# Kernel tuning notes

Measured on AMD Instinct MI355X. Metric: run time of the kernel, lower is better.

Reference implementation:

```python
import jax, jax.numpy as jnp
import numpy as np

MIN_NORM = 1e-15
EPS = 1e-7
N_NODES = 100000
N_EDGES = 1600000
D_IN = 256
D_OUT = 128

# ---- Hyperboloid manifold ops (HGCN-style) ----

def proj_tan0(u, c):
    # zero out the time (first) coordinate
    return jnp.concatenate([jnp.zeros_like(u[..., :1]), u[..., 1:]], axis=-1)

def proj(x, c):
    # project onto hyperboloid: recompute time coord from space coords
    K = 1.0 / c
    y = x[..., 1:]
    t = jnp.sqrt(jnp.clip(K + jnp.sum(y * y, axis=-1, keepdims=True), EPS, None))
    return jnp.concatenate([t, y], axis=-1)

def expmap0(u, c):
    sqrtK = jnp.sqrt(1.0 / c)
    x = u[..., 1:]
    nrm = jnp.clip(jnp.linalg.norm(x, axis=-1, keepdims=True), MIN_NORM, None)
    theta = nrm / sqrtK
    t0 = sqrtK * jnp.cosh(theta)
    rest = sqrtK * jnp.sinh(theta) * x / nrm
    return proj(jnp.concatenate([t0, rest], axis=-1), c)

def logmap0(x, c):
    sqrtK = jnp.sqrt(1.0 / c)
    y = x[..., 1:]
    nrm = jnp.clip(jnp.linalg.norm(y, axis=-1, keepdims=True), MIN_NORM, None)
    theta = jnp.clip(x[..., :1] / sqrtK, 1.0 + EPS, None)
    rest = sqrtK * jnp.arccosh(theta) * y / nrm
    return jnp.concatenate([jnp.zeros_like(rest[..., :1]), rest], axis=-1)

def mobius_matvec1(m, x, c):
    # weight is (in, out): map via tangent space at origin
    return expmap0(logmap0(x, c) @ m, c)

def mobius_matvec0(n, x, c):
    # per-node scalar (N,1) scaling in tangent space
    return expmap0(n * logmap0(x, c), c)

def mobius_add(x, y, c):
    # tangent-space addition at origin (broadcasts over bias rows)
    return expmap0(logmap0(x, c) + logmap0(y, c), c)

mobius_add0 = mobius_add

def spmm(rows, cols, vals, x):
    # COO sparse adj @ dense x  ->  [N, d]
    return jax.ops.segment_sum(vals[:, None] * x[cols], rows, num_segments=N_NODES)

def gcn_layer(x, weight, bias, rows, cols, vals, c):
    out = mobius_matvec1(weight, x, c)
    hyp_bias = proj(expmap0(proj_tan0(bias[None, :], c), c), c)
    out = mobius_add(out, hyp_bias, c)
    out = logmap0(out, c)
    out = spmm(rows, cols, vals, out)
    return proj(expmap0(out, c), c)


def setup_inputs() -> dict:
    key = jax.random.key(0)
    ks = jax.random.split(key, 12)
    A1_tensor = jax.random.normal(ks[0], (N_NODES, D_IN), dtype=jnp.float32)
    adj_rows = jax.random.randint(ks[1], (N_EDGES,), 0, N_NODES)
    adj_cols = jax.random.randint(ks[2], (N_EDGES,), 0, N_NODES)
    adj_vals = jax.random.uniform(ks[3], (N_EDGES,), dtype=jnp.float32) / 16.0
    raw_c = jnp.full((1,), np.log(np.e - 1.0), dtype=jnp.float32)
    bnd_in = 1.0 / np.sqrt(D_IN)
    bnd_h = 1.0 / np.sqrt(D_OUT)
    Lin1 = jax.random.uniform(ks[4], (D_IN, D_OUT), jnp.float32, -bnd_in, bnd_in)
    Lin1_bias = jax.random.uniform(ks[5], (D_OUT,), jnp.float32, -bnd_in, bnd_in)
    n = jax.random.uniform(ks[6], (N_NODES, 1), jnp.float32, 0.0, 1.0)
    gc1_weight = jax.random.uniform(ks[7], (D_IN, D_OUT), jnp.float32, -bnd_in, bnd_in)
    gc1_bias = jax.random.uniform(ks[8], (D_OUT,), jnp.float32, -bnd_in, bnd_in)
    gc2_weight = jax.random.uniform(ks[9], (D_OUT, D_OUT), jnp.float32, -bnd_h, bnd_h)
    gc2_bias = jax.random.uniform(ks[10], (D_OUT,), jnp.float32, -bnd_h, bnd_h)
    return {"A1_tensor": A1_tensor, "adj_rows": adj_rows, "adj_cols": adj_cols,
            "adj_vals": adj_vals, "raw_c": raw_c, "Lin1": Lin1, "Lin1_bias": Lin1_bias,
            "n": n, "gc1_weight": gc1_weight, "gc1_bias": gc1_bias,
            "gc2_weight": gc2_weight, "gc2_bias": gc2_bias}


def reference(A1_tensor, adj_rows, adj_cols, adj_vals, raw_c, Lin1, Lin1_bias, n,
              gc1_weight, gc1_bias, gc2_weight, gc2_bias):
    c = jax.nn.softplus(raw_c) + 1e-5  # learned curvature, shape (1,)
    # dropout is identity at inference
    x_tan = proj_tan0(A1_tensor, c)
    a = proj(expmap0(x_tan, c), c)
    # skip branch: hyperbolic linear
    a1 = mobius_matvec1(Lin1, a, c)
    hyp_bias = proj(expmap0(proj_tan0(Lin1_bias[None, :], c), c), c)
    a1 = mobius_add(a1, hyp_bias, c)
    a2 = mobius_matvec0(n, a1, c)
    # GCN layer 1 + gated residual
    x_1 = gcn_layer(a, gc1_weight, gc1_bias, adj_rows, adj_cols, adj_vals, c)
    x_1 = mobius_matvec0(1.0 - n, x_1, c)
    x_1 = mobius_add0(x_1, a2, c)
    # GCN layer 2
    x_2 = gcn_layer(x_1, gc2_weight, gc2_bias, adj_rows, adj_cols, adj_vals, c)
    x_2 = logmap0(x_2, c)
    x_2 = jnp.concatenate([x_2, a1], axis=-1)  # [N, 2*D_OUT]
    x_2 = expmap0(x_2, c)
    return (x_2, c)
```

## Files before the change

### kernel.cpp

```cpp
#include <hip/hip_runtime.h>
#include <math.h>


#define NN 100000
#define NP 100096
#define MAXDEG 64
#define NB 391
#define CAP 5120
#define EPT 8
#define EPB 2048

typedef __attribute__((ext_vector_type(8))) short bf16x8;
typedef __attribute__((ext_vector_type(4))) float f32x4;

__device__ __forceinline__ float wsum(float v) {
#pragma unroll
  for (int off = 32; off > 0; off >>= 1) v += __shfl_xor(v, off, 64);
  return v;
}

__device__ __forceinline__ float sane(float v) {
  return fminf(fmaxf(v, -3.0e38f), 3.0e38f);
}

__device__ __forceinline__ float b2f(ushort h) {
  union { unsigned u; float f; } z; z.u = (unsigned)h << 16; return z.f;
}
__device__ __forceinline__ ushort f2b(float f) {
  union { float f; unsigned u; } z; z.f = f;
  unsigned u = z.u;
  unsigned r = (u + 0x7fffu + ((u >> 16) & 1u)) >> 16;
  return (ushort)r;
}

__device__ __forceinline__ void gload16(const void* g, void* l) {
  __builtin_amdgcn_global_load_lds((const __attribute__((address_space(1))) void*)g,
                                   (__attribute__((address_space(3))) void*)l, 16, 0, 0);
}

__global__ __launch_bounds__(256) void prep_kernel(const float* __restrict__ Lin1,
                                                   const float* __restrict__ g1w,
                                                   const float* __restrict__ g2w,
                                                   ushort* __restrict__ Bt1,
                                                   ushort* __restrict__ Btg1,
                                                   ushort* __restrict__ Btg2,
                                                   int* __restrict__ bucketCnt,
                                                   const float* __restrict__ raw_c,
                                                   float* __restrict__ SC,
                                                   ushort* __restrict__ TBh) {
  int i = blockIdx.x * 256 + threadIdx.x;
  if (i < 32768) {
    int k = i >> 7, n = i & 127;
    Bt1[n * 256 + k] = f2b(Lin1[i]);
  } else if (i < 65536) {
    int j = i - 32768, k = j >> 7, n = j & 127;
    Btg1[n * 256 + k] = f2b(g1w[j]);
  } else if (i < 81920) {
    int j = i - 65536, k = j >> 7, n = j & 127;
    Btg2[n * 128 + k] = f2b(g2w[j]);
  } else if (i < 81920 + NB) {
    bucketCnt[i - 81920] = 0;
  } else if (i == 81920 + NB) {
    float rc = raw_c[0];
    float c = fmaxf(rc, 0.0f) + log1pf(expf(-fabsf(rc))) + 1e-5f;
    SC[0] = c;
    SC[1] = 1.0f / c;
    SC[2] = sqrtf(1.0f / c);
    SC[3] = sqrtf(c);
  } else if (i >= 90000 && i < 90000 + 6144) {
    ((unsigned*)(TBh + (size_t)NN * 128))[i - 90000] = 0u;
  }
}

__global__ __launch_bounds__(256) void convA_kernel(const float* __restrict__ A1,
                                                    ushort* __restrict__ A1h) {
  long i = (long)blockIdx.x * 256 + threadIdx.x;
  const long total = (long)NP * 32;
  if (i >= total) return;
  long row = i >> 5;
  if (row >= NN) {
    uint4 z = make_uint4(0, 0, 0, 0);
    *(uint4*)(A1h + i * 8) = z;
    return;
  }
  const float* p = A1 + i * 8;
  float4 v0 = *(const float4*)p;
  float4 v1 = *(const float4*)(p + 4);
  ushort t[8] = {f2b(v0.x), f2b(v0.y), f2b(v0.z), f2b(v0.w),
                 f2b(v1.x), f2b(v1.y), f2b(v1.z), f2b(v1.w)};
  if (((i * 8) & 255) == 0) t[0] = 0;
  *(uint4*)(A1h + i * 8) = *(uint4*)t;
}

__global__ __launch_bounds__(256) void mfma_gemm_kernel(const ushort* __restrict__ A, int lda,
                                                        const ushort* __restrict__ Bt,
                                                        ushort* __restrict__ C,
                                                        const float* __restrict__ bias,
                                                        int K) {
  __shared__ ushort As[128 * 32];
  __shared__ ushort Bs[128 * 32];
  const int tid = threadIdx.x;
  const int w = tid >> 6, l = tid & 63;
  const int wr = w >> 1, wc = w & 1;
  const int lane16 = l & 15, quad = l >> 4;
  const int bm = blockIdx.x * 128;
  const int swz = (lane16 >> 1) & 3;
  f32x4 acc[4][4];
#pragma unroll
  for (int mt = 0; mt < 4; ++mt)
#pragma unroll
    for (int nt = 0; nt < 4; ++nt) acc[mt][nt] = (f32x4){0.f, 0.f, 0.f, 0.f};

  for (int k0 = 0; k0 < K; k0 += 32) {
#pragma unroll
    for (int p = 0; p < 2; ++p) {
      int sseg = p * 256 + tid;
      int row = sseg >> 2;
      int kq = (sseg & 3) ^ ((row >> 1) & 3);
      int wbase = (p * 256 + (tid & ~63)) * 16;
      gload16(A + (size_t)(bm + row) * lda + k0 + kq * 8, (char*)As + wbase);
      gload16(Bt + (size_t)row * K + k0 + kq * 8, (char*)Bs + wbase);
    }
    __syncthreads();
    bf16x8 af[4], bfr[4];
#pragma unroll
    for (int mt = 0; mt < 4; ++mt)
      af[mt] = *(const bf16x8*)((const char*)As +
                (size_t)(wr * 64 + mt * 16 + lane16) * 64 + ((quad ^ swz) * 16));
#pragma unroll
    for (int nt = 0; nt < 4; ++nt)
      bfr[nt] = *(const bf16x8*)((const char*)Bs +
                 (size_t)(wc * 64 + nt * 16 + lane16) * 64 + ((quad ^ swz) * 16));
#pragma unroll
    for (int mt = 0; mt < 4; ++mt)
#pragma unroll
      for (int nt = 0; nt < 4; ++nt)
        acc[mt][nt] = __builtin_amdgcn_mfma_f32_16x16x32_bf16(bfr[nt], af[mt], acc[mt][nt], 0, 0, 0);
    __syncthreads();
  }
#pragma unroll
  for (int nt = 0; nt < 4; ++nt) {
    int colb = wc * 64 + nt * 16 + quad * 4;
    float4 b4 = *(const float4*)(bias + colb);
    if (colb == 0) b4.x = 0.0f;
#pragma unroll
    for (int mt = 0; mt < 4; ++mt) {
      int row = bm + wr * 64 + mt * 16 + lane16;
      ushort4 st;
      st.x = f2b(acc[mt][nt][0] + b4.x);
      st.y = f2b(acc[mt][nt][1] + b4.y);
      st.z = f2b(acc[mt][nt][2] + b4.z);
      st.w = f2b(acc[mt][nt][3] + b4.w);
      *(ushort4*)(C + (size_t)row * 128 + colb) = st;
    }
  }
}

__global__ __launch_bounds__(256) void part1_kernel(const int* __restrict__ rows,
                                                    const int* __restrict__ cols,
                                                    const float* __restrict__ vals,
                                                    int* __restrict__ bucketCnt,
                                                    uint2* __restrict__ store, int E) {
  __shared__ int hist[NB];
  __shared__ int cursor[NB];
  const int tid = threadIdx.x;
  for (int t = tid; t < NB; t += 256) hist[t] = 0;
  __syncthreads();
  const long base = (long)blockIdx.x * EPB;
  int rw[EPT], ck[EPT];
  float vf[EPT];
#pragma unroll
  for (int k = 0; k < EPT; ++k) {
    long i = base + (long)k * 256 + tid;
    rw[k] = -1;
    if (i < E) { rw[k] = rows[i]; ck[k] = cols[i]; vf[k] = vals[i]; }
  }
#pragma unroll
  for (int k = 0; k < EPT; ++k)
    if (rw[k] >= 0) atomicAdd(&hist[rw[k] >> 8], 1);
  __syncthreads();
  for (int t = tid; t < NB; t += 256) {
    int h = hist[t];
    cursor[t] = (h > 0) ? atomicAdd(&bucketCnt[t], h) : 0;
  }
  __syncthreads();
#pragma unroll
  for (int k = 0; k < EPT; ++k) {
    if (rw[k] >= 0) {
      int b = rw[k] >> 8;
      int pos = atomicAdd(&cursor[b], 1);
      unsigned pk = ((unsigned)ck[k] << 15) | ((unsigned)f2b(vf[k]) & 0x7FFFu);
      if (pos < CAP) store[(size_t)b * CAP + pos] = make_uint2(pk, (unsigned)rw[k]);
    }
  }
}

__global__ __launch_bounds__(1024) void part2_kernel(const int* __restrict__ bucketCnt,
                                                     const uint2* __restrict__ store,
                                                     int* __restrict__ deg,
                                                     unsigned* __restrict__ eCV) {
  __shared__ int d2[256];
  const int b = blockIdx.x, tid = threadIdx.x;
  if (tid < 256) d2[tid] = 0;
  __syncthreads();
  int n = bucketCnt[b];
  n = (n > CAP) ? CAP : n;
  const uint2* bs = store + (size_t)b * CAP;
  for (int i = tid; i < n; i += 1024) {
    uint2 rec = bs[i];
    int rl = rec.y & 255;
    int k = atomicAdd(&d2[rl], 1);
    if (k < MAXDEG) eCV[((size_t)rec.y << 6) + k] = rec.x;
  }
  __syncthreads();
  if (tid < 256) {
    int gr = b * 256 + tid;
    if (gr < NN) {
      int dgv = d2[tid];
      dgv = (dgv > MAXDEG) ? MAXDEG : dgv;
      int pe = (dgv + 15) & ~15;
      for (int k = dgv; k < pe; ++k) eCV[((size_t)gr << 6) + k] = 0u;
      deg[gr] = pe;
    }
  }
}

__device__ __forceinline__ void row_gather(int row, int l,
                                           const int* __restrict__ deg,
                                           const unsigned* __restrict__ eCV,
                                           const ushort* __restrict__ Gh,
                                           float& a0, float& a1) {
  unsigned mine = eCV[(size_t)row * MAXDEG + l];
  int dg = __builtin_amdgcn_readfirstlane(deg[row]);
  a0 = 0.0f; a1 = 0.0f;
  const int lo = l << 1;
  for (int j = 0; j < dg; j += 16) {
    unsigned pj[16];
    ushort2 u[16];
#pragma unroll
    for (int q = 0; q < 16; ++q) {
      pj[q] = (unsigned)__builtin_amdgcn_readlane((int)mine, j + q);
      u[q] = *(const ushort2*)(Gh + ((size_t)(pj[q] >> 15) << 7) + lo);
    }
#pragma unroll
    for (int q = 0; q < 16; ++q) {
      union { unsigned u32; float f; } vv; vv.u32 = (pj[q] & 0x7FFFu) << 16;
      a0 = fmaf(vv.f, b2f(u[q].x), a0);
      a1 = fmaf(vv.f, b2f(u[q].y), a1);
    }
  }
}

__global__ __launch_bounds__(256) void spmm1_kernel(const int* __restrict__ deg,
                                                    const unsigned* __restrict__ eCV,
                                                    const ushort* __restrict__ G1h,
                                                    const ushort* __restrict__ Pb,
                                                    const float* __restrict__ nvec,
                                                    const float* __restrict__ SC,
                                                    ushort* __restrict__ TBh,
                                                    ushort* __restrict__ A1Ph) {
  int row = __builtin_amdgcn_readfirstlane(blockIdx.x * 4 + (threadIdx.x >> 6));
  int l = threadIdx.x & 63;
  if (row >= NN) return;
  float sK = SC[2], rsK = SC[3];
  float nval = nvec[row];
  float a0, a1;
  row_gather(row, l, deg, eCV, G1h, a0, a1);
  ushort2 pu = *(const ushort2*)(Pb + (size_t)row * 128 + 2 * l);
  float p0 = b2f(pu.x), p1 = b2f(pu.y);
  float t10 = (l == 0) ? 0.0f : fmaf(1.0f - nval, a0, nval * p0);
  float t11 = fmaf(1.0f - nval, a1, nval * p1);
  ushort2 tb; tb.x = f2b(t10); tb.y = f2b(t11);
  *(ushort2*)(TBh + (size_t)row * 128 + 2 * l) = tb;
  float px = (l == 0) ? 0.0f : p0;
  float py = p1;
  float ss = wsum(px * px + py * py);
  float rinv = fminf(__builtin_amdgcn_rsqf(ss), 1e15f);
  float nrm = ss * rinv;
  float th = nrm * rsK;
  float e = __expf(th);
  float ei = __builtin_amdgcn_rcpf(e);
  float sh = 0.5f * (e - ei), ch = 0.5f * (e + ei);
  float sc = sK * sh * rinv;
  float t = sK * ch;
  ushort2 st;
  st.x = f2b((l == 0) ? t : sc * px);
  st.y = f2b(sc * py);
  *(ushort2*)(A1Ph + (size_t)row * 128 + 2 * l) = st;
}

__global__ __launch_bounds__(256) void spmm2_kernel(const int* __restrict__ deg,
                                                    const unsigned* __restrict__ eCV,
                                                    const ushort* __restrict__ G2h,
                                                    const ushort* __restrict__ A1Ph,
                                                    const float* __restrict__ SC,
                                                    float* __restrict__ out) {
  int row = __builtin_amdgcn_readfirstlane(blockIdx.x * 4 + (threadIdx.x >> 6));
  int l = threadIdx.x & 63;
  if (row >= NN) return;
  float cval = SC[0], K = SC[1], sK = SC[2], rsK = SC[3];
  float a0, a1;
  row_gather(row, l, deg, eCV, G2h, a0, a1);
  float u0 = (l == 0) ? 0.0f : a0;
  float u1 = a1;
  ushort2 ap = *(const ushort2*)(A1Ph + (size_t)row * 128 + 2 * l);
  float u2 = b2f(ap.x), u3 = b2f(ap.y);
  float ss = wsum(u0 * u0 + u1 * u1 + u2 * u2 + u3 * u3);
  float rinv = fminf(__builtin_amdgcn_rsqf(ss), 1e15f);
  float nrm = ss * rinv;
  float th = nrm * rsK;
  float e = __expf(th);
  float ei = __builtin_amdgcn_rcpf(e);
  float sc = sK * (0.5f * (e - ei)) * rinv;
  float o0 = sc * u0, o1 = sc * u1, o2 = sc * u2, o3 = sc * u3;
  if (l == 0) o0 = 0.0f;
  float t2 = sqrtf(fmaxf(K + sc * sc * ss, 1e-7f));
  float* op = out + (size_t)row * 256;
  float2 w0, w1;
  w0.x = sane((l == 0) ? t2 : o0);
  w0.y = sane(o1);
  w1.x = sane(o2);
  w1.y = sane(o3);
  *(float2*)(op + 2 * l) = w0;
  *(float2*)(op + 128 + 2 * l) = w1;
  if (row == 0 && l == 0) out[(size_t)NN * 256] = cval;
}

extern "C" void kernel_launch(void* const* d_in, const int* in_sizes, int n_in,
                              void* d_out, int out_size, void* d_ws, size_t ws_size,
                              hipStream_t stream) {
  const float* A1  = (const float*)d_in[0];
  const int* rows  = (const int*)d_in[1];
  const int* cols  = (const int*)d_in[2];
  const float* vals = (const float*)d_in[3];
  const float* rawc = (const float*)d_in[4];
  const float* Lin1 = (const float*)d_in[5];
  const float* Lb   = (const float*)d_in[6];
  const float* nv   = (const float*)d_in[7];
  const float* g1w  = (const float*)d_in[8];
  const float* g1b  = (const float*)d_in[9];
  const float* g2w  = (const float*)d_in[10];
  const float* g2b  = (const float*)d_in[11];
  float* out = (float*)d_out;
  float* ws = (float*)d_ws;
  const int E = in_sizes[1];

  float*  SC   = ws;
  ushort* A1h  = (ushort*)(ws + 256);
  ushort* Pb   = A1h + (size_t)256 * NP;
  ushort* G1h  = Pb + (size_t)128 * NP;
  ushort* TBh  = G1h + (size_t)128 * NP;
  ushort* A1Ph = TBh + (size_t)128 * NP;
  ushort* Bt1  = A1Ph + (size_t)128 * NP;
  ushort* Btg1 = Bt1 + 128 * 256;
  ushort* Btg2 = Btg1 + 128 * 256;
  int* deg      = (int*)(Btg2 + 128 * 256);
  unsigned* eCV = (unsigned*)(deg + NP);
  uint2* store   = (uint2*)A1Ph;
  int* bucketCnt = (int*)(store + (size_t)NB * CAP);

  const int rowBlocks = NN / 4;
  const int gemmGrid = NP / 128;
  const int p1Blocks = (E + EPB - 1) / EPB;
  const int prepBlocks = (90000 + 6144 + 255) / 256;

  prep_kernel<<<prepBlocks, 256, 0, stream>>>(Lin1, g1w, g2w, Bt1, Btg1, Btg2,
                                              bucketCnt, rawc, SC, TBh);
  part1_kernel<<<p1Blocks, 256, 0, stream>>>(rows, cols, vals, bucketCnt, store, E);
  part2_kernel<<<NB, 1024, 0, stream>>>(bucketCnt, store, deg, eCV);

  convA_kernel<<<(NP * 32 + 255) / 256, 256, 0, stream>>>(A1, A1h);
  mfma_gemm_kernel<<<gemmGrid, 256, 0, stream>>>(A1h, 256, Bt1, Pb, Lb, 256);
  mfma_gemm_kernel<<<gemmGrid, 256, 0, stream>>>(A1h, 256, Btg1, G1h, g1b, 256);
  spmm1_kernel<<<rowBlocks, 256, 0, stream>>>(deg, eCV, G1h, Pb, nv, SC, TBh, A1Ph);
  mfma_gemm_kernel<<<gemmGrid, 256, 0, stream>>>(TBh, 128, Btg2, G1h, g2b, 128);
  spmm2_kernel<<<rowBlocks, 256, 0, stream>>>(deg, eCV, G1h, A1Ph, SC, out);
}
```

Measured before the change: 457.0 us.

## Fuse A1 bf16 conversion and both input GEMMs into one kernel

Removes the separate fp32-to-bf16 conversion kernel and the two GEMMs that each re-read the bf16 A1 copy. The replacement is a single 512-thread GEMM against a concatenated 256-column weight matrix. It converts A1 from fp32 in-register while staging it into LDS and routes the two output halves to Pb and G1h with their respective biases. This saves one 51MB write and two reads of the intermediate plus two launches, at the cost of a non-pipelined fp32 global load inside the k-loop.

```diff
diff --git a/kernel.cpp b/kernel.cpp
--- a/kernel.cpp
+++ b/kernel.cpp
@@ -41,20 +41,17 @@
 __global__ __launch_bounds__(256) void prep_kernel(const float* __restrict__ Lin1,
                                                    const float* __restrict__ g1w,
                                                    const float* __restrict__ g2w,
-                                                   ushort* __restrict__ Bt1,
-                                                   ushort* __restrict__ Btg1,
+                                                   ushort* __restrict__ Btcat,
                                                    ushort* __restrict__ Btg2,
                                                    int* __restrict__ bucketCnt,
                                                    const float* __restrict__ raw_c,
                                                    float* __restrict__ SC,
                                                    ushort* __restrict__ TBh) {
   int i = blockIdx.x * 256 + threadIdx.x;
-  if (i < 32768) {
-    int k = i >> 7, n = i & 127;
-    Bt1[n * 256 + k] = f2b(Lin1[i]);
-  } else if (i < 65536) {
-    int j = i - 32768, k = j >> 7, n = j & 127;
-    Btg1[n * 256 + k] = f2b(g1w[j]);
+  if (i < 65536) {
+    int k = i >> 8, n = i & 255;
+    float v = (n < 128) ? Lin1[k * 128 + n] : g1w[k * 128 + (n - 128)];
+    Btcat[n * 256 + k] = f2b(v);
   } else if (i < 81920) {
     int j = i - 65536, k = j >> 7, n = j & 127;
     Btg2[n * 128 + k] = f2b(g2w[j]);
@@ -72,24 +69,86 @@
   }
 }
 
-__global__ __launch_bounds__(256) void convA_kernel(const float* __restrict__ A1,
-                                                    ushort* __restrict__ A1h) {
-  long i = (long)blockIdx.x * 256 + threadIdx.x;
-  const long total = (long)NP * 32;
-  if (i >= total) return;
-  long row = i >> 5;
-  if (row >= NN) {
-    uint4 z = make_uint4(0, 0, 0, 0);
-    *(uint4*)(A1h + i * 8) = z;
-    return;
-  }
-  const float* p = A1 + i * 8;
-  float4 v0 = *(const float4*)p;
-  float4 v1 = *(const float4*)(p + 4);
-  ushort t[8] = {f2b(v0.x), f2b(v0.y), f2b(v0.z), f2b(v0.w),
-                 f2b(v1.x), f2b(v1.y), f2b(v1.z), f2b(v1.w)};
-  if (((i * 8) & 255) == 0) t[0] = 0;
-  *(uint4*)(A1h + i * 8) = *(uint4*)t;
+__global__ __launch_bounds__(512) void fused_gemm_kernel(const float* __restrict__ A1,
+                                                         const ushort* __restrict__ Btcat,
+                                                         ushort* __restrict__ Pb,
+                                                         ushort* __restrict__ G1h,
+                                                         const float* __restrict__ Lb,
+                                                         const float* __restrict__ g1b) {
+  __shared__ ushort As[128 * 32];
+  __shared__ ushort Bs[256 * 32];
+  const int tid = threadIdx.x;
+  const int w = tid >> 6, l = tid & 63;
+  const int wr = w >> 2, wc = w & 3;
+  const int lane16 = l & 15, quad = l >> 4;
+  const int bm = blockIdx.x * 128;
+  const int swz = (lane16 >> 1) & 3;
+  const int ar = tid >> 2;
+  const int ak = tid & 3;
+  const int akq = ak ^ ((ar >> 1) & 3);
+  const int grow = bm + ar;
+  f32x4 acc[4][4];
+#pragma unroll
+  for (int mt = 0; mt < 4; ++mt)
+#pragma unroll
+    for (int nt = 0; nt < 4; ++nt) acc[mt][nt] = (f32x4){0.f, 0.f, 0.f, 0.f};
+
+  for (int k0 = 0; k0 < 256; k0 += 32) {
+#pragma unroll
+    for (int p = 0; p < 2; ++p) {
+      int sseg = p * 512 + tid;
+      int row = sseg >> 2;
+      int kq = (sseg & 3) ^ ((row >> 1) & 3);
+      int wbase = (p * 512 + (tid & ~63)) * 16;
+      gload16(Btcat + (size_t)row * 256 + k0 + kq * 8, (char*)Bs + wbase);
+    }
+    float4 v0 = make_float4(0.f, 0.f, 0.f, 0.f);
+    float4 v1 = make_float4(0.f, 0.f, 0.f, 0.f);
+    if (grow < NN) {
+      const float* p = A1 + (size_t)grow * 256 + k0 + ak * 8;
+      v0 = *(const float4*)p;
+      v1 = *(const float4*)(p + 4);
+    }
+    if (k0 == 0 && ak == 0) v0.x = 0.0f;
+    ushort t8[8] = {f2b(v0.x), f2b(v0.y), f2b(v0.z), f2b(v0.w),
+                    f2b(v1.x), f2b(v1.y), f2b(v1.z), f2b(v1.w)};
+    *(uint4*)(As + ar * 32 + akq * 8) = *(uint4*)t8;
+    __syncthreads();
+    bf16x8 af[4], bfr[4];
+#pragma unroll
+    for (int mt = 0; mt < 4; ++mt)
+      af[mt] = *(const bf16x8*)((const char*)As +
+                (size_t)(wr * 64 + mt * 16 + lane16) * 64 + ((quad ^ swz) * 16));
+#pragma unroll
+    for (int nt = 0; nt < 4; ++nt)
+      bfr[nt] = *(const bf16x8*)((const char*)Bs +
+                 (size_t)(wc * 64 + nt * 16 + lane16) * 64 + ((quad ^ swz) * 16));
+#pragma unroll
+    for (int mt = 0; mt < 4; ++mt)
+#pragma unroll
+      for (int nt = 0; nt < 4; ++nt)
+        acc[mt][nt] = __builtin_amdgcn_mfma_f32_16x16x32_bf16(bfr[nt], af[mt], acc[mt][nt], 0, 0, 0);
+    __syncthreads();
+  }
+#pragma unroll
+  for (int nt = 0; nt < 4; ++nt) {
+    int colb = wc * 64 + nt * 16 + quad * 4;
+    bool isP = colb < 128;
+    int cl = isP ? colb : colb - 128;
+    float4 b4 = *(const float4*)((isP ? Lb : g1b) + cl);
+    if (cl == 0) b4.x = 0.0f;
+    ushort* Cp = isP ? Pb : G1h;
+#pragma unroll
+    for (int mt = 0; mt < 4; ++mt) {
+      int row = bm + wr * 64 + mt * 16 + lane16;
+      ushort4 st;
+      st.x = f2b(acc[mt][nt][0] + b4.x);
+      st.y = f2b(acc[mt][nt][1] + b4.y);
+      st.z = f2b(acc[mt][nt][2] + b4.z);
+      st.w = f2b(acc[mt][nt][3] + b4.w);
+      *(ushort4*)(Cp + (size_t)row * 128 + cl) = st;
+    }
+  }
 }
 
 __global__ __launch_bounds__(256) void mfma_gemm_kernel(const ushort* __restrict__ A, int lda,
@@ -346,15 +405,13 @@
   const int E = in_sizes[1];
 
   float*  SC   = ws;
-  ushort* A1h  = (ushort*)(ws + 256);
-  ushort* Pb   = A1h + (size_t)256 * NP;
+  ushort* Pb   = (ushort*)(ws + 256);
   ushort* G1h  = Pb + (size_t)128 * NP;
   ushort* TBh  = G1h + (size_t)128 * NP;
   ushort* A1Ph = TBh + (size_t)128 * NP;
-  ushort* Bt1  = A1Ph + (size_t)128 * NP;
-  ushort* Btg1 = Bt1 + 128 * 256;
-  ushort* Btg2 = Btg1 + 128 * 256;
-  int* deg      = (int*)(Btg2 + 128 * 256);
+  ushort* Btcat = A1Ph + (size_t)128 * NP;
+  ushort* Btg2 = Btcat + 256 * 256;
+  int* deg      = (int*)(Btg2 + 128 * 128);
   unsigned* eCV = (unsigned*)(deg + NP);
   uint2* store   = (uint2*)A1Ph;
   int* bucketCnt = (int*)(store + (size_t)NB * CAP);
@@ -364,14 +421,12 @@
   const int p1Blocks = (E + EPB - 1) / EPB;
   const int prepBlocks = (90000 + 6144 + 255) / 256;
 
-  prep_kernel<<<prepBlocks, 256, 0, stream>>>(Lin1, g1w, g2w, Bt1, Btg1, Btg2,
+  prep_kernel<<<prepBlocks, 256, 0, stream>>>(Lin1, g1w, g2w, Btcat, Btg2,
                                               bucketCnt, rawc, SC, TBh);
   part1_kernel<<<p1Blocks, 256, 0, stream>>>(rows, cols, vals, bucketCnt, store, E);
   part2_kernel<<<NB, 1024, 0, stream>>>(bucketCnt, store, deg, eCV);
 
-  convA_kernel<<<(NP * 32 + 255) / 256, 256, 0, stream>>>(A1, A1h);
-  mfma_gemm_kernel<<<gemmGrid, 256, 0, stream>>>(A1h, 256, Bt1, Pb, Lb, 256);
-  mfma_gemm_kernel<<<gemmGrid, 256, 0, stream>>>(A1h, 256, Btg1, G1h, g1b, 256);
+  fused_gemm_kernel<<<gemmGrid, 512, 0, stream>>>(A1, Btcat, Pb, G1h, Lb, g1b);
   spmm1_kernel<<<rowBlocks, 256, 0, stream>>>(deg, eCV, G1h, Pb, nv, SC, TBh, A1Ph);
   mfma_gemm_kernel<<<gemmGrid, 256, 0, stream>>>(TBh, 128, Btg2, G1h, g2b, 128);
   spmm2_kernel<<<rowBlocks, 256, 0, stream>>>(deg, eCV, G1h, A1Ph, SC, out);
```

Result: faster. 427.8 us (-6.4%).
